# Performance work log

Measured on AMD Instinct MI355X. Metric: run time of the kernel, lower is better.

## Reference

```python
import jax, jax.numpy as jnp
import numpy as np

D = 85  # label-distribution length -> selects A3 branch

def _build_A(d):
    if d == 5:
        base = jnp.arange(5)
        return 1.0 - jnp.abs(base[:, None] - base[None, :]) / 5.0
    if d == 10:
        base = jnp.arange(10)
        return 1.0 - jnp.abs(base[:, None] - base[None, :]) / 10.0
    base = jnp.arange(85)
    return (1.0 - jnp.abs(base[:, None] - base[None, :]) / 85.0).astype(jnp.float32)

def setup_inputs() -> dict:
    key = jax.random.key(0)
    k1, k2 = jax.random.split(key)
    B = 262144
    inp = jax.random.normal(k1, (B, D), dtype=jnp.float32)
    tgt = jax.random.uniform(k2, (B, D), dtype=jnp.float32)
    return {"input": inp, "target": tgt}

def reference(input, target):
    A = _build_A(input.shape[1]).astype(input.dtype)
    diff = jnp.abs(input - target)            # [B, d]
    # per-row quadratic form diff_i^T A diff_i, summed over batch
    q = jnp.einsum('bi,ij,bj->b', diff, A, diff)
    return 0.1 * q.sum()
```

## Files before the change

### kernel.cpp

```cpp
#include <hip/hip_runtime.h>
#include <hip/hip_bf16.h>


#define QFD_D 85
#define ROWS_PER_BLOCK 64
#define THREADS 256

#define F4_VALID 1360
#define ROUNDS 22

typedef __attribute__((address_space(1))) const void glob_cv;
typedef __attribute__((address_space(3))) void lds_v;

__global__ __launch_bounds__(THREADS) void qfd_kernel(
    const float* __restrict__ in, const float* __restrict__ tgt,
    float* __restrict__ partial) {
    __shared__ float lin[ROUNDS * 256];
    __shared__ float ltg[ROUNDS * 256];
    __shared__ float wsum[THREADS / 64];

    const int tid  = threadIdx.x;
    const int lane = tid & 63;
    const int wave = tid >> 6;
    const int base4 = blockIdx.x * F4_VALID;

    const float4* in4 = reinterpret_cast<const float4*>(in) + base4;
    const float4* tg4 = reinterpret_cast<const float4*>(tgt) + base4;

    for (int r = wave; r < ROUNDS; r += 4) {
        int idx = r * 64 + lane;
        int g = idx < F4_VALID ? idx : 0;
        __builtin_amdgcn_global_load_lds(
            (glob_cv*)(in4 + g), (lds_v*)&lin[r * 256], 16, 0, 0);
        __builtin_amdgcn_global_load_lds(
            (glob_cv*)(tg4 + g), (lds_v*)&ltg[r * 256], 16, 0, 0);
    }
    __syncthreads();

    const int q   = tid & 3;
    const int row = tid >> 2;
    const int off = 21 * q + (q != 0);
    const int p   = row * QFD_D + off;

    float l = 0.0f, a1 = 0.0f, b2 = 0.0f;
    #pragma unroll
    for (int j = 0; j < 21; ++j) {
        float v = fabsf(lin[p + j] - ltg[p + j]);
        l += v;
        a1 += l;
        b2 = fmaf(l, l, b2);
    }
    if (q == 0) {
        float v = fabsf(lin[p + 21] - ltg[p + 21]);
        l += v;
        a1 += l;
        b2 = fmaf(l, l, b2);
    }

    const int qb = lane & 60;
    float s0 = __shfl(l, qb + 0, 64);
    float s1 = __shfl(l, qb + 1, 64);
    float s2 = __shfl(l, qb + 2, 64);
    float s3 = __shfl(l, qb + 3, 64);
    float S  = (s0 + s1) + (s2 + s3);
    float P  = (q > 0 ? s0 : 0.0f) + (q > 1 ? s1 : 0.0f) + (q > 2 ? s2 : 0.0f);
    float len = (q == 0) ? 22.0f : 21.0f;
    float c1 = fmaf(len, P, a1);
    float c2 = fmaf(len * P, P, fmaf(2.0f * P, a1, b2));
    float c1s = __shfl(c1, qb + 0, 64) + __shfl(c1, qb + 1, 64)
              + __shfl(c1, qb + 2, 64) + __shfl(c1, qb + 3, 64);
    float c2s = __shfl(c2, qb + 0, 64) + __shfl(c2, qb + 1, 64)
              + __shfl(c2, qb + 2, 64) + __shfl(c2, qb + 3, 64);
    float sumL  = c1s - S;
    float sumL2 = c2s - S * S;
    float qrow  = fmaf(S, S, -(2.0f / 85.0f) * (S * sumL - sumL2));
    float val   = (q == 0) ? qrow : 0.0f;

    #pragma unroll
    for (int m = 32; m > 0; m >>= 1)
        val += __shfl_xor(val, m, 64);
    if (lane == 0) wsum[wave] = val;
    __syncthreads();
    if (tid == 0) {
        float s = 0.0f;
        #pragma unroll
        for (int w = 0; w < THREADS / 64; ++w) s += wsum[w];
        partial[blockIdx.x] = s;
    }
}

__global__ __launch_bounds__(THREADS) void qfd_reduce_kernel(
    const float* __restrict__ partial, float* __restrict__ out, int n) {
    __shared__ float wsum[THREADS / 64];
    const int tid = threadIdx.x;
    float s = 0.0f;
    for (int i = tid; i < n; i += THREADS) s += partial[i];
    #pragma unroll
    for (int m = 32; m > 0; m >>= 1)
        s += __shfl_xor(s, m, 64);
    if ((tid & 63) == 0) wsum[tid >> 6] = s;
    __syncthreads();
    if (tid == 0) {
        float t = 0.0f;
        #pragma unroll
        for (int w = 0; w < THREADS / 64; ++w) t += wsum[w];
        out[0] = 0.1f * t;
    }
}

extern "C" void kernel_launch(void* const* d_in, const int* in_sizes, int n_in,
                              void* d_out, int out_size, void* d_ws, size_t ws_size,
                              hipStream_t stream) {
    const float* in  = (const float*)d_in[0];
    const float* tgt = (const float*)d_in[1];
    float* out = (float*)d_out;
    float* partial = (float*)d_ws;

    const int B = in_sizes[0] / QFD_D;
    const int grid = B / ROWS_PER_BLOCK;

    qfd_kernel<<<grid, THREADS, 0, stream>>>(in, tgt, partial);
    qfd_reduce_kernel<<<1, THREADS, 0, stream>>>(partial, out, grid);
}
```

Baseline: 193.2 us.

## Convert to persistent grid with double-buffered async LDS prefetch

Replaces the one-block-per-64-rows launch with a persistent grid of 768 blocks of 128 threads. Each block loops over 32-row chunks and prefetches the next chunk into a second LDS buffer with global_load_lds while it computes the current one. The aim is to overlap memory loads with compute and to cut block launch overhead and the size of the partial-sum array. The risk is lower occupancy and less memory parallelism, with only one chunk in flight per block and a barrier each iteration.

```diff
diff --git a/kernel.cpp b/kernel.cpp
--- a/kernel.cpp
+++ b/kernel.cpp
@@ -1,81 +1,109 @@
 #include <hip/hip_runtime.h>
-#include <hip/hip_bf16.h>
 
 
 #define QFD_D 85
-#define ROWS_PER_BLOCK 64
-#define THREADS 256
-
-#define F4_VALID 1360
-#define ROUNDS 22
+#define ROWS_PER_CHUNK 32
+#define THREADS 128
+#define NWAVES (THREADS / 64)
+#define F4_PER_CHUNK 680
+#define ROUNDS 11
+#define BUF_FLOATS (ROUNDS * 256)
 
 typedef __attribute__((address_space(1))) const void glob_cv;
 typedef __attribute__((address_space(3))) void lds_v;
 
 __global__ __launch_bounds__(THREADS) void qfd_kernel(
     const float* __restrict__ in, const float* __restrict__ tgt,
-    float* __restrict__ partial) {
-    __shared__ float lin[ROUNDS * 256];
-    __shared__ float ltg[ROUNDS * 256];
-    __shared__ float wsum[THREADS / 64];
+    float* __restrict__ partial, int nchunks) {
+    __shared__ float lin[2][BUF_FLOATS];
+    __shared__ float ltg[2][BUF_FLOATS];
+    __shared__ float wsum[NWAVES];
 
     const int tid  = threadIdx.x;
     const int lane = tid & 63;
     const int wave = tid >> 6;
-    const int base4 = blockIdx.x * F4_VALID;
 
-    const float4* in4 = reinterpret_cast<const float4*>(in) + base4;
-    const float4* tg4 = reinterpret_cast<const float4*>(tgt) + base4;
-
-    for (int r = wave; r < ROUNDS; r += 4) {
-        int idx = r * 64 + lane;
-        int g = idx < F4_VALID ? idx : 0;
-        __builtin_amdgcn_global_load_lds(
-            (glob_cv*)(in4 + g), (lds_v*)&lin[r * 256], 16, 0, 0);
-        __builtin_amdgcn_global_load_lds(
-            (glob_cv*)(tg4 + g), (lds_v*)&ltg[r * 256], 16, 0, 0);
-    }
-    __syncthreads();
+    const float4* in4 = reinterpret_cast<const float4*>(in);
+    const float4* tg4 = reinterpret_cast<const float4*>(tgt);
 
     const int q   = tid & 3;
     const int row = tid >> 2;
     const int off = 21 * q + (q != 0);
     const int p   = row * QFD_D + off;
+    const int qb  = lane & 60;
+    const float len = (q == 0) ? 22.0f : 21.0f;
 
-    float l = 0.0f, a1 = 0.0f, b2 = 0.0f;
-    #pragma unroll
-    for (int j = 0; j < 21; ++j) {
-        float v = fabsf(lin[p + j] - ltg[p + j]);
-        l += v;
-        a1 += l;
-        b2 = fmaf(l, l, b2);
+    float acc = 0.0f;
+
+    {
+        const float4* ia = in4 + (long)blockIdx.x * F4_PER_CHUNK;
+        const float4* ta = tg4 + (long)blockIdx.x * F4_PER_CHUNK;
+        for (int r = wave; r < ROUNDS; r += NWAVES) {
+            int idx = r * 64 + lane;
+            int g = idx < F4_PER_CHUNK ? idx : 0;
+            __builtin_amdgcn_global_load_lds(
+                (glob_cv*)(ia + g), (lds_v*)&lin[0][r * 256], 16, 0, 0);
+            __builtin_amdgcn_global_load_lds(
+                (glob_cv*)(ta + g), (lds_v*)&ltg[0][r * 256], 16, 0, 0);
+        }
     }
-    if (q == 0) {
-        float v = fabsf(lin[p + 21] - ltg[p + 21]);
-        l += v;
-        a1 += l;
-        b2 = fmaf(l, l, b2);
+    __syncthreads();
+
+    int cur = 0;
+    for (int c = blockIdx.x; c < nchunks; c += gridDim.x) {
+        const int cn = c + (int)gridDim.x;
+        if (cn < nchunks) {
+            const float4* ia = in4 + (long)cn * F4_PER_CHUNK;
+            const float4* ta = tg4 + (long)cn * F4_PER_CHUNK;
+            for (int r = wave; r < ROUNDS; r += NWAVES) {
+                int idx = r * 64 + lane;
+                int g = idx < F4_PER_CHUNK ? idx : 0;
+                __builtin_amdgcn_global_load_lds(
+                    (glob_cv*)(ia + g), (lds_v*)&lin[cur ^ 1][r * 256], 16, 0, 0);
+                __builtin_amdgcn_global_load_lds(
+                    (glob_cv*)(ta + g), (lds_v*)&ltg[cur ^ 1][r * 256], 16, 0, 0);
+            }
+        }
+
+        const float* Li = &lin[cur][0];
+        const float* Lt = &ltg[cur][0];
+        float l = 0.0f, a1 = 0.0f, b2 = 0.0f;
+        #pragma unroll
+        for (int j = 0; j < 21; ++j) {
+            float v = fabsf(Li[p + j] - Lt[p + j]);
+            l += v;
+            a1 += l;
+            b2 = fmaf(l, l, b2);
+        }
+        if (q == 0) {
+            float v = fabsf(Li[p + 21] - Lt[p + 21]);
+            l += v;
+            a1 += l;
+            b2 = fmaf(l, l, b2);
+        }
+
+        float s0 = __shfl(l, qb + 0, 64);
+        float s1 = __shfl(l, qb + 1, 64);
+        float s2 = __shfl(l, qb + 2, 64);
+        float s3 = __shfl(l, qb + 3, 64);
+        float S  = (s0 + s1) + (s2 + s3);
+        float P  = (q > 0 ? s0 : 0.0f) + (q > 1 ? s1 : 0.0f) + (q > 2 ? s2 : 0.0f);
+        float c1 = fmaf(len, P, a1);
+        float c2 = fmaf(len * P, P, fmaf(2.0f * P, a1, b2));
+        float c1s = __shfl(c1, qb + 0, 64) + __shfl(c1, qb + 1, 64)
+                  + __shfl(c1, qb + 2, 64) + __shfl(c1, qb + 3, 64);
+        float c2s = __shfl(c2, qb + 0, 64) + __shfl(c2, qb + 1, 64)
+                  + __shfl(c2, qb + 2, 64) + __shfl(c2, qb + 3, 64);
+        float sumL  = c1s - S;
+        float sumL2 = c2s - S * S;
+        float qrow  = fmaf(S, S, -(2.0f / 85.0f) * (S * sumL - sumL2));
+        if (q == 0) acc += qrow;
+
+        __syncthreads();
+        cur ^= 1;
     }
 
-    const int qb = lane & 60;
-    float s0 = __shfl(l, qb + 0, 64);
-    float s1 = __shfl(l, qb + 1, 64);
-    float s2 = __shfl(l, qb + 2, 64);
-    float s3 = __shfl(l, qb + 3, 64);
-    float S  = (s0 + s1) + (s2 + s3);
-    float P  = (q > 0 ? s0 : 0.0f) + (q > 1 ? s1 : 0.0f) + (q > 2 ? s2 : 0.0f);
-    float len = (q == 0) ? 22.0f : 21.0f;
-    float c1 = fmaf(len, P, a1);
-    float c2 = fmaf(len * P, P, fmaf(2.0f * P, a1, b2));
-    float c1s = __shfl(c1, qb + 0, 64) + __shfl(c1, qb + 1, 64)
-              + __shfl(c1, qb + 2, 64) + __shfl(c1, qb + 3, 64);
-    float c2s = __shfl(c2, qb + 0, 64) + __shfl(c2, qb + 1, 64)
-              + __shfl(c2, qb + 2, 64) + __shfl(c2, qb + 3, 64);
-    float sumL  = c1s - S;
-    float sumL2 = c2s - S * S;
-    float qrow  = fmaf(S, S, -(2.0f / 85.0f) * (S * sumL - sumL2));
-    float val   = (q == 0) ? qrow : 0.0f;
-
+    float val = acc;
     #pragma unroll
     for (int m = 32; m > 0; m >>= 1)
         val += __shfl_xor(val, m, 64);
@@ -84,14 +112,14 @@
     if (tid == 0) {
         float s = 0.0f;
         #pragma unroll
-        for (int w = 0; w < THREADS / 64; ++w) s += wsum[w];
+        for (int w = 0; w < NWAVES; ++w) s += wsum[w];
         partial[blockIdx.x] = s;
     }
 }
 
 __global__ __launch_bounds__(THREADS) void qfd_reduce_kernel(
     const float* __restrict__ partial, float* __restrict__ out, int n) {
-    __shared__ float wsum[THREADS / 64];
+    __shared__ float wsum[NWAVES];
     const int tid = threadIdx.x;
     float s = 0.0f;
     for (int i = tid; i < n; i += THREADS) s += partial[i];
@@ -103,7 +131,7 @@
     if (tid == 0) {
         float t = 0.0f;
         #pragma unroll
-        for (int w = 0; w < THREADS / 64; ++w) t += wsum[w];
+        for (int w = 0; w < NWAVES; ++w) t += wsum[w];
         out[0] = 0.1f * t;
     }
 }
@@ -117,8 +145,10 @@
     float* partial = (float*)d_ws;
 
     const int B = in_sizes[0] / QFD_D;
-    const int grid = B / ROWS_PER_BLOCK;
+    const int nchunks = B / ROWS_PER_CHUNK;
+    int grid = 256 * 3;
+    if (grid > nchunks) grid = nchunks;
 
-    qfd_kernel<<<grid, THREADS, 0, stream>>>(in, tgt, partial);
+    qfd_kernel<<<grid, THREADS, 0, stream>>>(in, tgt, partial, nchunks);
     qfd_reduce_kernel<<<1, THREADS, 0, stream>>>(partial, out, grid);
 }
```

Result: no change. 194.6 us (+0.7%).

## Replace LDS staging with one-row-per-thread direct global loads, software-pipelined

Applied to the files above, without the earlier changes.

Drops the global_load_lds staging of 64 rows per block into shared memory and the 4-lanes-per-row split with shuffle combining. Each thread now owns a whole 85-float row and streams it from global memory in 12-float groups through a rotating three-buffer register pipeline, which removes the LDS round trip, the block barrier and the cross-lane fix-up. The cost is strided, uncoalesced per-thread access, since each lane reads its own 340-byte row using 4-byte-aligned vector loads. It also uses many more registers per thread, and the 256-row blocks reduce the number of partial sums.

```diff
diff --git a/kernel.cpp b/kernel.cpp
--- a/kernel.cpp
+++ b/kernel.cpp
@@ -1,81 +1,74 @@
 #include <hip/hip_runtime.h>
-#include <hip/hip_bf16.h>
 
 
 #define QFD_D 85
-#define ROWS_PER_BLOCK 64
 #define THREADS 256
+#define NWAVES (THREADS / 64)
 
-#define F4_VALID 1360
-#define ROUNDS 22
+typedef float f4a __attribute__((ext_vector_type(4), aligned(4)));
 
-typedef __attribute__((address_space(1))) const void glob_cv;
-typedef __attribute__((address_space(3))) void lds_v;
-
-__global__ __launch_bounds__(THREADS) void qfd_kernel(
+__global__ __launch_bounds__(THREADS, 4) void qfd_kernel(
     const float* __restrict__ in, const float* __restrict__ tgt,
-    float* __restrict__ partial) {
-    __shared__ float lin[ROUNDS * 256];
-    __shared__ float ltg[ROUNDS * 256];
-    __shared__ float wsum[THREADS / 64];
-
+    float* __restrict__ partial, int B) {
+    __shared__ float wsum[NWAVES];
     const int tid  = threadIdx.x;
     const int lane = tid & 63;
     const int wave = tid >> 6;
-    const int base4 = blockIdx.x * F4_VALID;
+    const int row  = blockIdx.x * THREADS + tid;
 
-    const float4* in4 = reinterpret_cast<const float4*>(in) + base4;
-    const float4* tg4 = reinterpret_cast<const float4*>(tgt) + base4;
+    float qrow = 0.0f;
+    if (row < B) {
+        const float* pi = in  + (size_t)row * QFD_D;
+        const float* pt = tgt + (size_t)row * QFD_D;
 
-    for (int r = wave; r < ROUNDS; r += 4) {
-        int idx = r * 64 + lane;
-        int g = idx < F4_VALID ? idx : 0;
-        __builtin_amdgcn_global_load_lds(
-            (glob_cv*)(in4 + g), (lds_v*)&lin[r * 256], 16, 0, 0);
-        __builtin_amdgcn_global_load_lds(
-            (glob_cv*)(tg4 + g), (lds_v*)&ltg[r * 256], 16, 0, 0);
-    }
-    __syncthreads();
+        float l = 0.0f, a1 = 0.0f, b2 = 0.0f;
 
-    const int q   = tid & 3;
-    const int row = tid >> 2;
-    const int off = 21 * q + (q != 0);
-    const int p   = row * QFD_D + off;
+#define LOADG(SI0,SI1,SI2,ST0,ST1,ST2,g)          \
+        SI0 = *(const f4a*)(pi + 12*(g));         \
+        SI1 = *(const f4a*)(pi + 12*(g) + 4);     \
+        SI2 = *(const f4a*)(pi + 12*(g) + 8);     \
+        ST0 = *(const f4a*)(pt + 12*(g));         \
+        ST1 = *(const f4a*)(pt + 12*(g) + 4);     \
+        ST2 = *(const f4a*)(pt + 12*(g) + 8);
 
-    float l = 0.0f, a1 = 0.0f, b2 = 0.0f;
-    #pragma unroll
-    for (int j = 0; j < 21; ++j) {
-        float v = fabsf(lin[p + j] - ltg[p + j]);
-        l += v;
-        a1 += l;
-        b2 = fmaf(l, l, b2);
-    }
-    if (q == 0) {
-        float v = fabsf(lin[p + 21] - ltg[p + 21]);
-        l += v;
-        a1 += l;
-        b2 = fmaf(l, l, b2);
+#define C1(vi,vt) { float v = fabsf((vi) - (vt)); l += v; a1 += l; b2 = fmaf(l, l, b2); }
+#define CONSG(SI0,SI1,SI2,ST0,ST1,ST2)                                    \
+        C1(SI0.x,ST0.x) C1(SI0.y,ST0.y) C1(SI0.z,ST0.z) C1(SI0.w,ST0.w)   \
+        C1(SI1.x,ST1.x) C1(SI1.y,ST1.y) C1(SI1.z,ST1.z) C1(SI1.w,ST1.w)   \
+        C1(SI2.x,ST2.x) C1(SI2.y,ST2.y) C1(SI2.z,ST2.z) C1(SI2.w,ST2.w)
+
+        f4a Ai0,Ai1,Ai2, At0,At1,At2;
+        f4a Bi0,Bi1,Bi2, Bt0,Bt1,Bt2;
+        f4a Ci0,Ci1,Ci2, Ct0,Ct1,Ct2;
+
+        float e84i = pi[84];
+        float e84t = pt[84];
+        LOADG(Ai0,Ai1,Ai2,At0,At1,At2, 0)
+        LOADG(Bi0,Bi1,Bi2,Bt0,Bt1,Bt2, 1)
+        LOADG(Ci0,Ci1,Ci2,Ct0,Ct1,Ct2, 2)
+        CONSG(Ai0,Ai1,Ai2,At0,At1,At2)
+        LOADG(Ai0,Ai1,Ai2,At0,At1,At2, 3)
+        CONSG(Bi0,Bi1,Bi2,Bt0,Bt1,Bt2)
+        LOADG(Bi0,Bi1,Bi2,Bt0,Bt1,Bt2, 4)
+        CONSG(Ci0,Ci1,Ci2,Ct0,Ct1,Ct2)
+        LOADG(Ci0,Ci1,Ci2,Ct0,Ct1,Ct2, 5)
+        CONSG(Ai0,Ai1,Ai2,At0,At1,At2)
+        LOADG(Ai0,Ai1,Ai2,At0,At1,At2, 6)
+        CONSG(Bi0,Bi1,Bi2,Bt0,Bt1,Bt2)
+        CONSG(Ci0,Ci1,Ci2,Ct0,Ct1,Ct2)
+        CONSG(Ai0,Ai1,Ai2,At0,At1,At2)
+        C1(e84i, e84t)
+
+        float S = l;
+        float sumL  = a1 - S;
+        float sumL2 = b2 - S * S;
+        qrow = fmaf(S, S, -(2.0f / 85.0f) * (S * sumL - sumL2));
+#undef LOADG
+#undef C1
+#undef CONSG
     }
 
-    const int qb = lane & 60;
-    float s0 = __shfl(l, qb + 0, 64);
-    float s1 = __shfl(l, qb + 1, 64);
-    float s2 = __shfl(l, qb + 2, 64);
-    float s3 = __shfl(l, qb + 3, 64);
-    float S  = (s0 + s1) + (s2 + s3);
-    float P  = (q > 0 ? s0 : 0.0f) + (q > 1 ? s1 : 0.0f) + (q > 2 ? s2 : 0.0f);
-    float len = (q == 0) ? 22.0f : 21.0f;
-    float c1 = fmaf(len, P, a1);
-    float c2 = fmaf(len * P, P, fmaf(2.0f * P, a1, b2));
-    float c1s = __shfl(c1, qb + 0, 64) + __shfl(c1, qb + 1, 64)
-              + __shfl(c1, qb + 2, 64) + __shfl(c1, qb + 3, 64);
-    float c2s = __shfl(c2, qb + 0, 64) + __shfl(c2, qb + 1, 64)
-              + __shfl(c2, qb + 2, 64) + __shfl(c2, qb + 3, 64);
-    float sumL  = c1s - S;
-    float sumL2 = c2s - S * S;
-    float qrow  = fmaf(S, S, -(2.0f / 85.0f) * (S * sumL - sumL2));
-    float val   = (q == 0) ? qrow : 0.0f;
-
+    float val = qrow;
     #pragma unroll
     for (int m = 32; m > 0; m >>= 1)
         val += __shfl_xor(val, m, 64);
@@ -84,14 +77,14 @@
     if (tid == 0) {
         float s = 0.0f;
         #pragma unroll
-        for (int w = 0; w < THREADS / 64; ++w) s += wsum[w];
+        for (int w = 0; w < NWAVES; ++w) s += wsum[w];
         partial[blockIdx.x] = s;
     }
 }
 
 __global__ __launch_bounds__(THREADS) void qfd_reduce_kernel(
     const float* __restrict__ partial, float* __restrict__ out, int n) {
-    __shared__ float wsum[THREADS / 64];
+    __shared__ float wsum[NWAVES];
     const int tid = threadIdx.x;
     float s = 0.0f;
     for (int i = tid; i < n; i += THREADS) s += partial[i];
@@ -103,7 +96,7 @@
     if (tid == 0) {
         float t = 0.0f;
         #pragma unroll
-        for (int w = 0; w < THREADS / 64; ++w) t += wsum[w];
+        for (int w = 0; w < NWAVES; ++w) t += wsum[w];
         out[0] = 0.1f * t;
     }
 }
@@ -117,8 +110,8 @@
     float* partial = (float*)d_ws;
 
     const int B = in_sizes[0] / QFD_D;
-    const int grid = B / ROWS_PER_BLOCK;
+    const int grid = (B + THREADS - 1) / THREADS;
 
-    qfd_kernel<<<grid, THREADS, 0, stream>>>(in, tgt, partial);
+    qfd_kernel<<<grid, THREADS, 0, stream>>>(in, tgt, partial, B);
     qfd_reduce_kernel<<<1, THREADS, 0, stream>>>(partial, out, grid);
 }
```

Measured after the change: 218.7 us. +13.2%, slower.

## Shrink blocks to a single wave of 16 rows and drop block-level reduction

Applied to the files above, without the earlier changes.

Each block now has one 64-thread wave handling 16 rows instead of four waves handling 64 rows. The LDS staging loop is fully unrolled, and the partial sum is written straight from lane 0 without shared memory or a block barrier. The aim is more independent blocks with less LDS each, so more can be resident and loads overlap better. In exchange there are four times more blocks and partials, and the single-block final reduction has to sum 16384 values.

```diff
diff --git a/kernel.cpp b/kernel.cpp
--- a/kernel.cpp
+++ b/kernel.cpp
@@ -1,13 +1,13 @@
 #include <hip/hip_runtime.h>
-#include <hip/hip_bf16.h>
 
 
 #define QFD_D 85
-#define ROWS_PER_BLOCK 64
-#define THREADS 256
+#define ROWS_PER_BLOCK 16
+#define THREADS 64
 
-#define F4_VALID 1360
-#define ROUNDS 22
+#define F4_VALID 340
+#define ROUNDS 6
+#define BUF_FLOATS (ROUNDS * 256)
 
 typedef __attribute__((address_space(1))) const void glob_cv;
 typedef __attribute__((address_space(3))) void lds_v;
@@ -15,19 +15,16 @@
 __global__ __launch_bounds__(THREADS) void qfd_kernel(
     const float* __restrict__ in, const float* __restrict__ tgt,
     float* __restrict__ partial) {
-    __shared__ float lin[ROUNDS * 256];
-    __shared__ float ltg[ROUNDS * 256];
-    __shared__ float wsum[THREADS / 64];
-
-    const int tid  = threadIdx.x;
-    const int lane = tid & 63;
-    const int wave = tid >> 6;
-    const int base4 = blockIdx.x * F4_VALID;
+    __shared__ float lin[BUF_FLOATS];
+    __shared__ float ltg[BUF_FLOATS];
+    const int lane = threadIdx.x;
+    const long base4 = (long)blockIdx.x * F4_VALID;
 
     const float4* in4 = reinterpret_cast<const float4*>(in) + base4;
     const float4* tg4 = reinterpret_cast<const float4*>(tgt) + base4;
 
-    for (int r = wave; r < ROUNDS; r += 4) {
+    #pragma unroll
+    for (int r = 0; r < ROUNDS; ++r) {
         int idx = r * 64 + lane;
         int g = idx < F4_VALID ? idx : 0;
         __builtin_amdgcn_global_load_lds(
@@ -37,8 +34,8 @@
     }
     __syncthreads();
 
-    const int q   = tid & 3;
-    const int row = tid >> 2;
+    const int q   = lane & 3;
+    const int row = lane >> 2;
     const int off = 21 * q + (q != 0);
     const int p   = row * QFD_D + off;
 
@@ -79,22 +76,15 @@
     #pragma unroll
     for (int m = 32; m > 0; m >>= 1)
         val += __shfl_xor(val, m, 64);
-    if (lane == 0) wsum[wave] = val;
-    __syncthreads();
-    if (tid == 0) {
-        float s = 0.0f;
-        #pragma unroll
-        for (int w = 0; w < THREADS / 64; ++w) s += wsum[w];
-        partial[blockIdx.x] = s;
-    }
+    if (lane == 0) partial[blockIdx.x] = val;
 }
 
-__global__ __launch_bounds__(THREADS) void qfd_reduce_kernel(
+__global__ __launch_bounds__(256) void qfd_reduce_kernel(
     const float* __restrict__ partial, float* __restrict__ out, int n) {
-    __shared__ float wsum[THREADS / 64];
+    __shared__ float wsum[4];
     const int tid = threadIdx.x;
     float s = 0.0f;
-    for (int i = tid; i < n; i += THREADS) s += partial[i];
+    for (int i = tid; i < n; i += 256) s += partial[i];
     #pragma unroll
     for (int m = 32; m > 0; m >>= 1)
         s += __shfl_xor(s, m, 64);
@@ -103,7 +93,7 @@
     if (tid == 0) {
         float t = 0.0f;
         #pragma unroll
-        for (int w = 0; w < THREADS / 64; ++w) t += wsum[w];
+        for (int w = 0; w < 4; ++w) t += wsum[w];
         out[0] = 0.1f * t;
     }
 }
@@ -120,5 +110,5 @@
     const int grid = B / ROWS_PER_BLOCK;
 
     qfd_kernel<<<grid, THREADS, 0, stream>>>(in, tgt, partial);
-    qfd_reduce_kernel<<<1, THREADS, 0, stream>>>(partial, out, grid);
+    qfd_reduce_kernel<<<1, 256, 0, stream>>>(partial, out, grid);
 }
```

Result: slower. 204.4 us (+5.8%).
